# Kernel tuning notes

Hardware: AMD Instinct MI355X
Metric: run time of the kernel (lower is better)

The kernel has to match this reference:

```python
import jax, jax.numpy as jnp
import numpy as np

B, S1, S2, H1, H2, HID = 8, 512, 512, 128, 128, 128

def setup_inputs() -> dict:
    key = jax.random.key(0)
    ks = jax.random.split(key, 8)
    return {
        "query": jax.random.normal(ks[0], (B, S1, H1), jnp.float32),
        "key": jax.random.normal(ks[1], (B, S2, H2), jnp.float32),
        "value": jax.random.normal(ks[2], (B, S2, H2), jnp.float32),
        "q_mask": jax.random.randint(ks[3], (B, S1), 0, 2, jnp.int32),
        "k_mask": jax.random.randint(ks[4], (B, S2), 0, 2, jnp.int32),
        # init_weights: Linear weight ~ N(0, 0.01), bias = 0
        "W1": jax.random.normal(ks[5], (HID, H1 + H2), jnp.float32) * 0.01,
        "b1": jnp.zeros((HID,), jnp.float32),
        "W2": jax.random.normal(ks[6], (1, HID), jnp.float32) * 0.01,
        "b2": jnp.zeros((1,), jnp.float32),
    }

def reference(query, key, value, q_mask, k_mask, W1, b1, W2, b2):
    h1 = query.shape[-1]
    # Linear on concat([q,k]) == q @ W1[:, :h1].T + k @ W1[:, h1:].T + b1
    qp = jnp.einsum('bsd,hd->bsh', query, W1[:, :h1]) + b1   # [B,S1,HID]
    kp = jnp.einsum('btd,hd->bth', key, W1[:, h1:])          # [B,S2,HID]
    h = jax.nn.relu(qp[:, :, None, :] + kp[:, None, :, :])   # [B,S1,S2,HID]
    s = jnp.einsum('bsth,h->bst', h, W2[0]) + b2[0]          # [B,S1,S2]
    mask = (q_mask[:, :, None] * k_mask[:, None, :]) > 0     # [B,S1,S2]
    A = jnp.where(mask, jnp.exp(s), 0.0)                     # masked_fill(-inf).exp()
    A_sum = jnp.clip(jnp.sum(A, axis=-1, keepdims=True), 2e-15, None)
    attn = A / A_sum
    return jnp.einsum('bst,btd->bsd', attn, value)           # [B,S1,H2]
```

## Files before the change

### kernel.cpp

```cpp
#include <hip/hip_runtime.h>

#define S 512
#define H 128
#define NROW 4096
#define TI 8

typedef _Float16 h2v __attribute__((ext_vector_type(2)));
#define BCH(x) __builtin_bit_cast(h2v, (x))

static __device__ __forceinline__ unsigned pkh(float a, float b) {
  h2v p; p.x = (_Float16)a; p.y = (_Float16)b;
  return __builtin_bit_cast(unsigned, p);
}

__global__ __launch_bounds__(256) void proj_kernel(
    const float* __restrict__ query, const float* __restrict__ key,
    const float* __restrict__ value,
    const float* __restrict__ W1, const float* __restrict__ b1,
    const float* __restrict__ W2,
    unsigned* __restrict__ qph, unsigned* __restrict__ kph,
    unsigned* __restrict__ vph, unsigned* __restrict__ w2h)
{
  __shared__ float w1t[64][130];
  const int bid = blockIdx.x;
  const int tid = threadIdx.x;

  if (bid >= 1024) {
    const int base = (bid - 1024) * 2048 + tid * 8;
    const float4 v0 = *(const float4*)(value + base);
    const float4 v1 = *(const float4*)(value + base + 4);
    uint4 o;
    o.x = pkh(v0.x, v0.y); o.y = pkh(v0.z, v0.w);
    o.z = pkh(v1.x, v1.y); o.w = pkh(v1.z, v1.w);
    *(uint4*)(vph + (base >> 1)) = o;
    return;
  }

  const bool isq = bid < 512;
  const float* __restrict__ src = isq ? query : key;
  const int rbase = (isq ? bid : bid - 512) * 8;
  const int off = isq ? 0 : 128;

  if (bid == 0 && tid < 64) {
    w2h[tid] = pkh(W2[2 * tid], W2[2 * tid + 1]);
  }

  const int w = __builtin_amdgcn_readfirstlane(tid >> 6);
  const int lane = tid & 63;
  const int r0 = rbase + w * 2;

  float acc[2][2];
  float2 bv = make_float2(0.f, 0.f);
  if (isq) bv = *(const float2*)(b1 + 2 * lane);
  acc[0][0] = bv.x; acc[0][1] = bv.y;
  acc[1][0] = bv.x; acc[1][1] = bv.y;

  for (int p = 0; p < 2; p++) {
    for (int idx = tid; idx < 128 * 16; idx += 256) {
      const int d4 = idx & 15, h = idx >> 4;
      const float4 v = *(const float4*)(W1 + h * 256 + off + p * 64 + d4 * 4);
      w1t[d4 * 4 + 0][h] = v.x;
      w1t[d4 * 4 + 1][h] = v.y;
      w1t[d4 * 4 + 2][h] = v.z;
      w1t[d4 * 4 + 3][h] = v.w;
    }
    __syncthreads();

    for (int dc = 0; dc < 64; dc += 8) {
      float qs[2][8];
      #pragma unroll
      for (int r = 0; r < 2; r++) {
        const float* sp = src + (size_t)(r0 + r) * H + p * 64 + dc;
        #pragma unroll
        for (int u = 0; u < 8; u++) qs[r][u] = sp[u];
      }
      #pragma unroll
      for (int dd = 0; dd < 8; dd++) {
        const float2 wv = *(const float2*)&w1t[dc + dd][2 * lane];
        #pragma unroll
        for (int r = 0; r < 2; r++) {
          acc[r][0] = __builtin_fmaf(qs[r][dd], wv.x, acc[r][0]);
          acc[r][1] = __builtin_fmaf(qs[r][dd], wv.y, acc[r][1]);
        }
      }
    }
    __syncthreads();
  }

  unsigned* __restrict__ dst = isq ? qph : kph;
  #pragma unroll
  for (int r = 0; r < 2; r++)
    dst[(size_t)(r0 + r) * 64 + lane] = pkh(acc[r][0], acc[r][1]);
}

__global__ __launch_bounds__(512, 4) void attn_kernel(
    const unsigned* __restrict__ qph, const unsigned* __restrict__ kph,
    const unsigned* __restrict__ w2h, const unsigned* __restrict__ vph,
    const int* __restrict__ q_mask, const int* __restrict__ k_mask,
    const float* __restrict__ b2, float* __restrict__ out)
{
  union __align__(16) SMU {
    float aT[8][64][12];
    float numk[8][TI][132];
  };
  __shared__ SMU sm;
  __shared__ float denk[8][TI];

  const int bid = blockIdx.x;
  const int it = (bid & 7) * 64 + (bid >> 3);
  const int r0 = it * TI;
  const int b = r0 >> 9;
  const int tid = threadIdx.x;
  const int w = __builtin_amdgcn_readfirstlane(tid >> 6);
  const int lane = tid & 63;
  const int jl = (w << 6) + lane;
  const int jg = (b << 9) + jl;
  const int km = k_mask[jg];
  const unsigned* __restrict__ kprow = kph + (size_t)jg * 64;
  const float b2v = b2[0];
  const h2v hz = {};

  int qmv[TI];
  int anyq = 0;
  #pragma unroll
  for (int i = 0; i < TI; i++) { qmv[i] = q_mask[r0 + i]; anyq |= qmv[i]; }

  float s[TI];
  #pragma unroll
  for (int i = 0; i < TI; i++) s[i] = 0.f;

  if (anyq) {
    for (int hc = 0; hc < 64; hc += 16) {
      h2v kr[16];
      {
        const uint4* k4 = (const uint4*)(kprow + hc);
        const uint4 a0 = k4[0], a1 = k4[1], a2 = k4[2], a3 = k4[3];
        kr[0]  = BCH(a0.x); kr[1]  = BCH(a0.y); kr[2]  = BCH(a0.z); kr[3]  = BCH(a0.w);
        kr[4]  = BCH(a1.x); kr[5]  = BCH(a1.y); kr[6]  = BCH(a1.z); kr[7]  = BCH(a1.w);
        kr[8]  = BCH(a2.x); kr[9]  = BCH(a2.y); kr[10] = BCH(a2.z); kr[11] = BCH(a2.w);
        kr[12] = BCH(a3.x); kr[13] = BCH(a3.y); kr[14] = BCH(a3.z); kr[15] = BCH(a3.w);
      }
      h2v w2c[16];
      #pragma unroll
      for (int u = 0; u < 16; u++) w2c[u] = BCH(w2h[hc + u]);

      #pragma unroll
      for (int i = 0; i < TI; i++) {
        if (qmv[i]) {
          const unsigned* __restrict__ qrow =
              qph + (size_t)(r0 + i) * 64 + hc;
          unsigned qu[16];
          #pragma unroll
          for (int u = 0; u < 16; u++) qu[u] = qrow[u];
          #pragma unroll
          for (int u = 0; u < 16; u++) {
            h2v t = BCH(qu[u]) + kr[u];
            t = __builtin_elementwise_max(t, hz);
            s[i] = __builtin_amdgcn_fdot2(t, w2c[u], s[i], false);
          }
        }
      }
    }
  }

  float a[TI];
  #pragma unroll
  for (int i = 0; i < TI; i++) {
    if (qmv[i]) {
      a[i] = (km > 0) ? __expf(s[i] + b2v) : 0.f;
      float d = a[i];
      #pragma unroll
      for (int m = 32; m >= 1; m >>= 1) d += __shfl_xor(d, m, 64);
      if (lane == 0) denk[w][i] = d;
    } else {
      a[i] = 0.f;
      if (lane == 0) denk[w][i] = 0.f;
    }
  }
  *(float4*)&sm.aT[w][lane][0] = make_float4(a[0], a[1], a[2], a[3]);
  *(float4*)&sm.aT[w][lane][4] = make_float4(a[4], a[5], a[6], a[7]);
  __syncthreads();

  const int lj = lane >> 5, lh = lane & 31;
  float nr[TI][4];
  #pragma unroll
  for (int i = 0; i < TI; i++) { nr[i][0]=0.f; nr[i][1]=0.f; nr[i][2]=0.f; nr[i][3]=0.f; }
  const unsigned* __restrict__ vbase =
      vph + ((size_t)b * S + (w << 6)) * 64;

  if (anyq) {
    #pragma unroll 4
    for (int js = 0; js < 32; js++) {
      const int j = js * 2 + lj;
      const uint2 vv = *(const uint2*)(vbase + (size_t)j * 64 + lh * 2);
      const h2v p0 = BCH(vv.x), p1 = BCH(vv.y);
      const float v0 = (float)p0.x, v1 = (float)p0.y;
      const float v2 = (float)p1.x, v3 = (float)p1.y;
      float av[TI];
      { const float4 t0 = *(const float4*)&sm.aT[w][j][0];
        const float4 t1 = *(const float4*)&sm.aT[w][j][4];
        av[0]=t0.x; av[1]=t0.y; av[2]=t0.z; av[3]=t0.w;
        av[4]=t1.x; av[5]=t1.y; av[6]=t1.z; av[7]=t1.w; }
      #pragma unroll
      for (int i = 0; i < TI; i++) {
        nr[i][0] = __builtin_fmaf(av[i], v0, nr[i][0]);
        nr[i][1] = __builtin_fmaf(av[i], v1, nr[i][1]);
        nr[i][2] = __builtin_fmaf(av[i], v2, nr[i][2]);
        nr[i][3] = __builtin_fmaf(av[i], v3, nr[i][3]);
      }
    }
    #pragma unroll
    for (int i = 0; i < TI; i++) {
      #pragma unroll
      for (int k = 0; k < 4; k++) nr[i][k] += __shfl_xor(nr[i][k], 32, 64);
    }
  }

  __syncthreads();
  if (lane < 32) {
    #pragma unroll
    for (int i = 0; i < TI; i++)
      *(float4*)&sm.numk[w][i][lane * 4] =
          make_float4(nr[i][0], nr[i][1], nr[i][2], nr[i][3]);
  }
  __syncthreads();

  const int ii = tid >> 6;
  const int h0 = tid & 63;
  float n0 = 0.f, n1 = 0.f, d = 0.f;
  #pragma unroll
  for (int ww = 0; ww < 8; ww++) {
    n0 += sm.numk[ww][ii][h0];
    n1 += sm.numk[ww][ii][h0 + 64];
    d += denk[ww][ii];
  }
  const float inv = 1.f / fmaxf(d, 2e-15f);
  out[(size_t)(r0 + ii) * H + h0] = n0 * inv;
  out[(size_t)(r0 + ii) * H + h0 + 64] = n1 * inv;
}

extern "C" void kernel_launch(void* const* d_in, const int* in_sizes, int n_in,
                              void* d_out, int out_size, void* d_ws, size_t ws_size,
                              hipStream_t stream)
{
  (void)in_sizes; (void)n_in; (void)out_size; (void)ws_size;
  const float* query  = (const float*)d_in[0];
  const float* key    = (const float*)d_in[1];
  const float* value  = (const float*)d_in[2];
  const int*   q_mask = (const int*)d_in[3];
  const int*   k_mask = (const int*)d_in[4];
  const float* W1     = (const float*)d_in[5];
  const float* b1     = (const float*)d_in[6];
  const float* W2     = (const float*)d_in[7];
  const float* b2     = (const float*)d_in[8];
  float* out = (float*)d_out;

  unsigned* ws  = (unsigned*)d_ws;
  unsigned* qph = ws;
  unsigned* kph = ws + (size_t)NROW * 64;
  unsigned* vph = kph + (size_t)NROW * 64;
  unsigned* w2h = vph + (size_t)NROW * 64;

  proj_kernel<<<1280, 256, 0, stream>>>(query, key, value, W1, b1, W2,
                                        qph, kph, vph, w2h);
  attn_kernel<<<512, 512, 0, stream>>>(qph, kph, w2h, vph, q_mask, k_mask,
                                       b2, out);
}
```

Measured before the change: 106.6 us.

## Compact live key columns per batch and skip fully masked waves

Builds a compacted list of unmasked key indices per block using ballot and popcount, so each wave processes only live keys and waves with no live keys skip both the score and the value accumulation loops. With random masks roughly half the keys are masked, so about half the waves skip their work. In exchange it adds two block-wide barriers, shared-memory index tables, and gathered (non-contiguous) loads of K and V rows through the index list.

```diff
diff --git a/kernel.cpp b/kernel.cpp
--- a/kernel.cpp
+++ b/kernel.cpp
@@ -105,6 +105,8 @@
   };
   __shared__ SMU sm;
   __shared__ float denk[8][TI];
+  __shared__ unsigned long long bm[8];
+  __shared__ unsigned short jorig[512];
 
   const int bid = blockIdx.x;
   const int it = (bid & 7) * 64 + (bid >> 3);
@@ -114,12 +116,31 @@
   const int w = __builtin_amdgcn_readfirstlane(tid >> 6);
   const int lane = tid & 63;
   const int jl = (w << 6) + lane;
-  const int jg = (b << 9) + jl;
-  const int km = k_mask[jg];
-  const unsigned* __restrict__ kprow = kph + (size_t)jg * 64;
   const float b2v = b2[0];
   const h2v hz = {};
 
+  const int kf = k_mask[(b << 9) + tid] > 0;
+  const unsigned long long m = __ballot(kf);
+  if (lane == 0) bm[w] = m;
+  __syncthreads();
+  int nlive = 0, basec = 0;
+  #pragma unroll
+  for (int x = 0; x < 8; x++) {
+    const int c = __popcll(bm[x]);
+    if (x < w) basec += c;
+    nlive += c;
+  }
+  if (kf) {
+    const int pos = basec + __popcll(m & ((1ull << lane) - 1));
+    jorig[pos] = (unsigned short)tid;
+  }
+  __syncthreads();
+
+  const bool live = jl < nlive;
+  const bool wlive = (w << 6) < nlive;
+  const int myj = live ? (int)jorig[jl] : 0;
+  const unsigned* __restrict__ kprow = kph + (size_t)((b << 9) + myj) * 64;
+
   int qmv[TI];
   int anyq = 0;
   #pragma unroll
@@ -129,7 +150,7 @@
   #pragma unroll
   for (int i = 0; i < TI; i++) s[i] = 0.f;
 
-  if (anyq) {
+  if (anyq && wlive) {
     for (int hc = 0; hc < 64; hc += 16) {
       h2v kr[16];
       {
@@ -166,11 +187,11 @@
   float a[TI];
   #pragma unroll
   for (int i = 0; i < TI; i++) {
-    if (qmv[i]) {
-      a[i] = (km > 0) ? __expf(s[i] + b2v) : 0.f;
+    if (qmv[i] && wlive) {
+      a[i] = live ? __expf(s[i] + b2v) : 0.f;
       float d = a[i];
       #pragma unroll
-      for (int m = 32; m >= 1; m >>= 1) d += __shfl_xor(d, m, 64);
+      for (int mm = 32; mm >= 1; mm >>= 1) d += __shfl_xor(d, mm, 64);
       if (lane == 0) denk[w][i] = d;
     } else {
       a[i] = 0.f;
@@ -185,17 +206,17 @@
   float nr[TI][4];
   #pragma unroll
   for (int i = 0; i < TI; i++) { nr[i][0]=0.f; nr[i][1]=0.f; nr[i][2]=0.f; nr[i][3]=0.f; }
-  const unsigned* __restrict__ vbase =
-      vph + ((size_t)b * S + (w << 6)) * 64;
-
-  if (anyq) {
+  const unsigned* __restrict__ vb = vph + (size_t)(b << 9) * 64;
+
+  if (anyq && wlive) {
     #pragma unroll 4
     for (int js = 0; js < 32; js++) {
       const int j = js * 2 + lj;
-      const uint2 vv = *(const uint2*)(vbase + (size_t)j * 64 + lh * 2);
-      const h2v p0 = BCH(vv.x), p1 = BCH(vv.y);
-      const float v0 = (float)p0.x, v1 = (float)p0.y;
-      const float v2 = (float)p1.x, v3 = (float)p1.y;
+      const int jr = __shfl(myj, j, 64);
+      const uint2 vv = *(const uint2*)(vb + (size_t)jr * 64 + lh * 2);
+      const h2v pv0 = BCH(vv.x), pv1 = BCH(vv.y);
+      const float v0 = (float)pv0.x, v1 = (float)pv0.y;
+      const float v2 = (float)pv1.x, v3 = (float)pv1.y;
       float av[TI];
       { const float4 t0 = *(const float4*)&sm.aT[w][j][0];
         const float4 t1 = *(const float4*)&sm.aT[w][j][4];
```

Result: no change. 104.6 us (-1.9%).
